# Performance work log

Measured on AMD Instinct MI355X. Metric: run time of the kernel, lower is better.

Reference implementation:

```python
import jax, jax.numpy as jnp
import numpy as np

F_DIM, H_DIM, B, T = 256, 512, 512, 128

def setup_inputs() -> dict:
    key = jax.random.key(0)
    ks = jax.random.split(key, 16)
    stdv_f = 1.0 / np.sqrt(F_DIM)
    stdv_h = 1.0 / np.sqrt(H_DIM)
    u = lambda k, shape, s: jax.random.uniform(k, shape, jnp.float32, -s, s)
    values = jax.random.normal(ks[0], (B, T, F_DIM), jnp.float32)
    delta = jax.random.uniform(ks[1], (B, T, F_DIM), jnp.float32) * 2.0
    masks = (jax.random.uniform(ks[2], (B, T, F_DIM)) < 0.8).astype(jnp.float32)
    inp = jnp.stack([values, delta, masks], axis=1)  # [B,3,T,F]
    return {
        'input': inp,
        # temp_decay_x (diag, F->F); mask buffer is unused in forward, faithful to source
        'Wdx': u(ks[3], (F_DIM, F_DIM), stdv_f), 'bdx': u(ks[4], (F_DIM,), stdv_f),
        # temp_decay_h (F->H)
        'Wdh': u(ks[5], (H_DIM, F_DIM), stdv_h), 'bdh': u(ks[6], (H_DIM,), stdv_h),
        # output_layer (H->F)
        'Wout': u(ks[7], (F_DIM, H_DIM), stdv_h), 'bout': u(ks[8], (F_DIM,), stdv_h),
        'Wz': u(ks[9], (F_DIM, F_DIM), stdv_f), 'bz': u(ks[10], (F_DIM,), stdv_f),
        # beta_layer (2F->F)
        'Wbeta': u(ks[11], (F_DIM, 2 * F_DIM), stdv_f), 'bbeta': u(ks[12], (F_DIM,), stdv_f),
        # GRUCell (2F -> H): weight_ih [3H,2F], weight_hh [3H,H]
        'Wih': u(ks[13], (3 * H_DIM, 2 * F_DIM), stdv_h),
        'Whh': u(ks[14], (3 * H_DIM, H_DIM), stdv_h),
        'bih': u(ks[15], (3 * H_DIM,), stdv_h),
        'bhh': u(jax.random.fold_in(key, 99), (3 * H_DIM,), stdv_h),
    }

def _mae(v, hat, m):
    return jnp.sum(jnp.abs(v - hat) * m) / (jnp.sum(m) + 1e-5)

def _forward(inp, Wdx, bdx, Wdh, bdh, Wout, bout, Wz, bz, Wbeta, bbeta, Wih, Whh, bih, bhh):
    values = jnp.transpose(inp[:, 0], (1, 0, 2))  # [T,B,F]
    delta = jnp.transpose(inp[:, 1], (1, 0, 2))
    masks = jnp.transpose(inp[:, 2], (1, 0, 2))
    H = Whh.shape[1]
    Wz_masked = Wz * (1.0 - jnp.eye(Wz.shape[0], dtype=Wz.dtype))

    def step(carry, xs):
        hid, loss = carry
        v, d, m = xs  # each [B,F]
        gamma_x = jnp.exp(-jax.nn.relu(d @ Wdx.T + bdx))
        gamma_h = jnp.exp(-jax.nn.relu(d @ Wdh.T + bdh))
        hid = hid * gamma_h
        x_hat = hid @ Wout.T + bout
        loss = loss + _mae(v, x_hat, m)
        x_c = m * v + (1.0 - m) * x_hat
        z_hat = x_c @ Wz_masked.T + bz
        loss = loss + _mae(v, z_hat, m)
        beta = jnp.concatenate([gamma_x, m], axis=1) @ Wbeta.T + bbeta
        c_hat = beta * z_hat + (1.0 - beta) * x_hat
        loss = loss + _mae(v, c_hat, m)
        c_c = m * v + (1.0 - m) * c_hat
        gi = jnp.concatenate([c_c, m], axis=1)  # [B,2F]
        gl = gi @ Wih.T + bih   # [B,3H]
        hl = hid @ Whh.T + bhh  # [B,3H]
        r = jax.nn.sigmoid(gl[:, :H] + hl[:, :H])
        z = jax.nn.sigmoid(gl[:, H:2 * H] + hl[:, H:2 * H])
        n = jnp.tanh(gl[:, 2 * H:] + r * hl[:, 2 * H:])
        hid = (1.0 - z) * n + z * hid
        return (hid, loss), (c_hat, c_c)

    hid0 = jnp.zeros((values.shape[1], H), dtype=inp.dtype)
    (_, x_loss), (c_hat_seq, c_c_seq) = jax.lax.scan(step, (hid0, jnp.float32(0.0)), (values, delta, masks))
    c_hat_list = jnp.transpose(c_hat_seq, (1, 0, 2))   # [B,T,F]
    imputations = jnp.transpose(c_c_seq, (1, 0, 2))    # [B,T,F]
    return c_hat_list, imputations, x_loss

def reference(input, Wdx, bdx, Wdh, bdh, Wout, bout, Wz, bz, Wbeta, bbeta, Wih, Whh, bih, bhh):
    return _forward(input, Wdx, bdx, Wdh, bdh, Wout, bout, Wz, bz, Wbeta, bbeta, Wih, Whh, bih, bhh)
```

## Files before the change

kernel.cpp:

```cpp
#include <hip/hip_runtime.h>
#include <math.h>


#define F 256
#define H 512
#define B 512
#define T 128
#define TF 32768
#define S3TF 98304
#define BTF ((size_t)B * T * F)

typedef __attribute__((ext_vector_type(8))) short bf8;
typedef __attribute__((ext_vector_type(4))) float f4;
#define MFMA16 __builtin_amdgcn_mfma_f32_16x16x32_bf16

__device__ inline short f2bf(float x) {
    unsigned u = __builtin_bit_cast(unsigned, x);
    u += 0x7fff + ((u >> 16) & 1);
    return (short)(u >> 16);
}
__device__ inline float bf2f(short s) {
    unsigned u = ((unsigned)(unsigned short)s) << 16;
    return __builtin_bit_cast(float, u);
}
__device__ inline float wsum(float v) {
#pragma unroll
    for (int o = 32; o > 0; o >>= 1) v += __shfl_down(v, o, 64);
    return v;
}

__global__ void init_k(float* __restrict__ hf, short* __restrict__ hb,
                       float* __restrict__ nd) {
    int i = blockIdx.x * 256 + threadIdx.x;
    hf[i] = 0.f; hb[i] = 0;
    if (i < 512) nd[i] = 0.f;
}

__global__ void wconv_k(const float* __restrict__ Wdx, const float* __restrict__ Wdh,
                        const float* __restrict__ Wz, const float* __restrict__ Wout,
                        const float* __restrict__ Wbeta, const float* __restrict__ Wih,
                        const float* __restrict__ Whh, short* __restrict__ wb) {
    int i = blockIdx.x * 256 + threadIdx.x;
    float v;
    if (i < 65536) v = Wdx[i];
    else if (i < 196608) v = Wdh[i - 65536];
    else if (i < 262144) { int l = i - 196608; v = ((l >> 8) == (l & 255)) ? 0.f : Wz[l]; }
    else if (i < 393216) v = Wout[i - 262144];
    else if (i < 524288) v = Wbeta[i - 393216];
    else if (i < 1310720) v = Wih[i - 524288];
    else v = Whh[i - 1310720];
    wb[i] = f2bf(v);
}

__global__ void aconv_k(const float* __restrict__ inp, short* __restrict__ dbf,
                        short* __restrict__ abf, float* __restrict__ den) {
    int i = blockIdx.x * 256 + threadIdx.x;
    int r = i >> 8, f = i & 255;
    int t = r >> 9, b = r & 511;
    const float* base = inp + (size_t)b * S3TF + (size_t)t * F;
    dbf[i] = f2bf(base[TF + f]);
    float m = base[2 * TF + f];
    abf[(size_t)r * 512 + 256 + f] = f2bf(m);
    float s = wsum(m);
    __shared__ float red[4];
    if ((threadIdx.x & 63) == 0) red[threadIdx.x >> 6] = s;
    __syncthreads();
    if (threadIdx.x == 0) atomicAdd(&den[t], red[0] + red[1] + red[2] + red[3]);
}

__global__ __launch_bounds__(256) void gx_gemm(const short* __restrict__ A,
                                               const short* __restrict__ W,
                                               const float* __restrict__ bias,
                                               short* __restrict__ abf) {
    int gw = blockIdx.x * 4 + (threadIdx.x >> 6);
    int lane = threadIdx.x & 63, l16 = lane & 15, quad = lane >> 4;
    int r0 = (gw >> 4) * 16, n0 = (gw & 15) * 16;
    const short* ar = A + (size_t)(r0 + l16) * 256 + quad * 8;
    const short* br = W + (size_t)(n0 + l16) * 256 + quad * 8;
    f4 acc = {};
#pragma unroll
    for (int k = 0; k < 256; k += 32)
        acc = MFMA16(*(const bf8*)(ar + k), *(const bf8*)(br + k), acc, 0, 0, 0);
    int n = n0 + l16;
    float bs = bias[n];
#pragma unroll
    for (int r = 0; r < 4; r++) {
        int row = r0 + quad * 4 + r;
        abf[(size_t)row * 512 + n] = f2bf(expf(-fmaxf(acc[r] + bs, 0.f)));
    }
}

__global__ __launch_bounds__(256) void gh_gemm(const short* __restrict__ A,
                                               const short* __restrict__ W,
                                               const float* __restrict__ bias,
                                               short* __restrict__ ghb) {
    int gw = blockIdx.x * 4 + (threadIdx.x >> 6);
    int lane = threadIdx.x & 63, l16 = lane & 15, quad = lane >> 4;
    int r0 = (gw >> 5) * 16, n0 = (gw & 31) * 16;
    const short* ar = A + (size_t)(r0 + l16) * 256 + quad * 8;
    const short* br = W + (size_t)(n0 + l16) * 256 + quad * 8;
    f4 acc = {};
#pragma unroll
    for (int k = 0; k < 256; k += 32)
        acc = MFMA16(*(const bf8*)(ar + k), *(const bf8*)(br + k), acc, 0, 0, 0);
    int n = n0 + l16;
    float bs = bias[n];
#pragma unroll
    for (int r = 0; r < 4; r++) {
        int row = r0 + quad * 4 + r;
        ghb[(size_t)row * 512 + n] = f2bf(expf(-fmaxf(acc[r] + bs, 0.f)));
    }
}

__global__ __launch_bounds__(256) void beta_gemm(const short* __restrict__ A,
                                                 const short* __restrict__ W,
                                                 const float* __restrict__ bias,
                                                 short* __restrict__ betab) {
    int gw = blockIdx.x * 4 + (threadIdx.x >> 6);
    int lane = threadIdx.x & 63, l16 = lane & 15, quad = lane >> 4;
    int r0 = (gw >> 4) * 16, n0 = (gw & 15) * 16;
    const short* ar = A + (size_t)(r0 + l16) * 512 + quad * 8;
    const short* br = W + (size_t)(n0 + l16) * 512 + quad * 8;
    f4 acc = {};
#pragma unroll
    for (int k = 0; k < 512; k += 32)
        acc = MFMA16(*(const bf8*)(ar + k), *(const bf8*)(br + k), acc, 0, 0, 0);
    int n = n0 + l16;
    float bs = bias[n];
#pragma unroll
    for (int r = 0; r < 4; r++) {
        int row = r0 + quad * 4 + r;
        betab[(size_t)row * 256 + n] = f2bf(acc[r] + bs);
    }
}

__global__ __launch_bounds__(256) void k1(const short* __restrict__ hidb,
                                          const short* __restrict__ Wo,
                                          const float* __restrict__ bout,
                                          const float* __restrict__ inp,
                                          short* __restrict__ xhatb,
                                          short* __restrict__ xcb,
                                          float* __restrict__ num, int t) {
    int gw = blockIdx.x * 4 + (threadIdx.x >> 6);
    int lane = threadIdx.x & 63, l16 = lane & 15, quad = lane >> 4;
    int b0 = (gw >> 4) * 16, n0 = (gw & 15) * 16;
    const short* ar = hidb + (size_t)(b0 + l16) * 512 + quad * 8;
    const short* br = Wo + (size_t)(n0 + l16) * 512 + quad * 8;
    f4 acc = {};
#pragma unroll
    for (int k = 0; k < 512; k += 32)
        acc = MFMA16(*(const bf8*)(ar + k), *(const bf8*)(br + k), acc, 0, 0, 0);
    int n = n0 + l16;
    float bs = bout[n];
    float l1 = 0.f;
#pragma unroll
    for (int r = 0; r < 4; r++) {
        int b = b0 + quad * 4 + r;
        const float* vb = inp + (size_t)b * S3TF + (size_t)t * F + n;
        float v = vb[0], m = vb[2 * TF];
        float xh = acc[r] + bs;
        l1 += fabsf(v - xh) * m;
        xhatb[(size_t)b * 256 + n] = f2bf(xh);
        xcb[(size_t)b * 256 + n] = f2bf(m * v + (1.f - m) * xh);
    }
    l1 = wsum(l1);
    __shared__ float red[4];
    if (lane == 0) red[threadIdx.x >> 6] = l1;
    __syncthreads();
    if (threadIdx.x == 0) atomicAdd(&num[t], red[0] + red[1] + red[2] + red[3]);
}

__global__ __launch_bounds__(256) void k2(const short* __restrict__ xcb,
                                          const short* __restrict__ Wzm,
                                          const float* __restrict__ bz,
                                          const short* __restrict__ xhatb,
                                          const short* __restrict__ betab,
                                          const float* __restrict__ inp,
                                          float* __restrict__ out,
                                          short* __restrict__ gib,
                                          float* __restrict__ num, int t) {
    int gw = blockIdx.x * 4 + (threadIdx.x >> 6);
    int lane = threadIdx.x & 63, l16 = lane & 15, quad = lane >> 4;
    int b0 = (gw >> 4) * 16, n0 = (gw & 15) * 16;
    const short* ar = xcb + (size_t)(b0 + l16) * 256 + quad * 8;
    const short* br = Wzm + (size_t)(n0 + l16) * 256 + quad * 8;
    f4 acc = {};
#pragma unroll
    for (int k = 0; k < 256; k += 32)
        acc = MFMA16(*(const bf8*)(ar + k), *(const bf8*)(br + k), acc, 0, 0, 0);
    int n = n0 + l16;
    float bs = bz[n];
    float l2 = 0.f, l3 = 0.f;
#pragma unroll
    for (int r = 0; r < 4; r++) {
        int b = b0 + quad * 4 + r;
        const float* vb = inp + (size_t)b * S3TF + (size_t)t * F + n;
        float v = vb[0], m = vb[2 * TF];
        float zh = acc[r] + bs;
        float xh = bf2f(xhatb[(size_t)b * 256 + n]);
        float bt = bf2f(betab[((size_t)t * 512 + b) * 256 + n]);
        float ch = bt * zh + (1.f - bt) * xh;
        float cc = m * v + (1.f - m) * ch;
        out[(size_t)b * TF + (size_t)t * F + n] = ch;
        out[BTF + (size_t)b * TF + (size_t)t * F + n] = cc;
        gib[(size_t)b * 512 + n] = f2bf(cc);
        gib[(size_t)b * 512 + 256 + n] = f2bf(m);
        l2 += fabsf(v - zh) * m;
        l3 += fabsf(v - ch) * m;
    }
    l2 = wsum(l2); l3 = wsum(l3);
    __shared__ float red2[2][4];
    if (lane == 0) { red2[0][threadIdx.x >> 6] = l2; red2[1][threadIdx.x >> 6] = l3; }
    __syncthreads();
    if (threadIdx.x == 0) {
        atomicAdd(&num[128 + t], red2[0][0] + red2[0][1] + red2[0][2] + red2[0][3]);
        atomicAdd(&num[256 + t], red2[1][0] + red2[1][1] + red2[1][2] + red2[1][3]);
    }
}

__global__ __launch_bounds__(256) void k3(const short* __restrict__ gib,
                                          const short* __restrict__ hidb,
                                          const float* __restrict__ hidf,
                                          const short* __restrict__ Wih,
                                          const short* __restrict__ Whh,
                                          const float* __restrict__ bih,
                                          const float* __restrict__ bhh,
                                          const short* __restrict__ ghb,
                                          float* __restrict__ hidf_n,
                                          short* __restrict__ hidb_n, int t) {
    int gw = blockIdx.x * 4 + (threadIdx.x >> 6);
    int lane = threadIdx.x & 63, l16 = lane & 15, quad = lane >> 4;
    int b0 = (gw >> 5) * 16, j0 = (gw & 31) * 16;
    const short* ag = gib + (size_t)(b0 + l16) * 512 + quad * 8;
    const short* ah = hidb + (size_t)(b0 + l16) * 512 + quad * 8;
    const short* w0 = Wih + (size_t)(j0 + l16) * 512 + quad * 8;
    const short* w3 = Whh + (size_t)(j0 + l16) * 512 + quad * 8;
    f4 aglr = {}, aglz = {}, agln = {}, ahlr = {}, ahlz = {}, ahln = {};
#pragma unroll
    for (int k = 0; k < 512; k += 32) {
        bf8 g = *(const bf8*)(ag + k);
        bf8 h = *(const bf8*)(ah + k);
        aglr = MFMA16(g, *(const bf8*)(w0 + k), aglr, 0, 0, 0);
        aglz = MFMA16(g, *(const bf8*)(w0 + 512 * 512 + k), aglz, 0, 0, 0);
        agln = MFMA16(g, *(const bf8*)(w0 + 1024 * 512 + k), agln, 0, 0, 0);
        ahlr = MFMA16(h, *(const bf8*)(w3 + k), ahlr, 0, 0, 0);
        ahlz = MFMA16(h, *(const bf8*)(w3 + 512 * 512 + k), ahlz, 0, 0, 0);
        ahln = MFMA16(h, *(const bf8*)(w3 + 1024 * 512 + k), ahln, 0, 0, 0);
    }
    int j = j0 + l16;
    float br = bih[j], bzg = bih[512 + j], bn = bih[1024 + j];
    float cr = bhh[j], czg = bhh[512 + j], cn = bhh[1024 + j];
#pragma unroll
    for (int r = 0; r < 4; r++) {
        int b = b0 + quad * 4 + r;
        float rg = 1.f / (1.f + expf(-(aglr[r] + br + ahlr[r] + cr)));
        float zg = 1.f / (1.f + expf(-(aglz[r] + bzg + ahlz[r] + czg)));
        float ng = tanhf(agln[r] + bn + rg * (ahln[r] + cn));
        float hold = hidf[(size_t)b * 512 + j];
        float hn = (1.f - zg) * ng + zg * hold;
        if (t + 1 < T) hn *= bf2f(ghb[((size_t)(t + 1) * 512 + b) * 512 + j]);
        hidf_n[(size_t)b * 512 + j] = hn;
        hidb_n[(size_t)b * 512 + j] = f2bf(hn);
    }
}

__global__ void final_k(const float* __restrict__ nd, float* __restrict__ outloss) {
    int tid = threadIdx.x;
    float v = (nd[tid] + nd[128 + tid] + nd[256 + tid]) / (nd[384 + tid] + 1e-5f);
    __shared__ float red[128];
    red[tid] = v; __syncthreads();
    for (int o = 64; o > 0; o >>= 1) { if (tid < o) red[tid] += red[tid + o]; __syncthreads(); }
    if (tid == 0) *outloss = red[0];
}

extern "C" void kernel_launch(void* const* d_in, const int* in_sizes, int n_in,
                              void* d_out, int out_size, void* d_ws, size_t ws_size,
                              hipStream_t stream) {
    const float* inp   = (const float*)d_in[0];
    const float* Wdx   = (const float*)d_in[1];
    const float* bdx   = (const float*)d_in[2];
    const float* Wdh   = (const float*)d_in[3];
    const float* bdh   = (const float*)d_in[4];
    const float* Wout  = (const float*)d_in[5];
    const float* bout  = (const float*)d_in[6];
    const float* Wz    = (const float*)d_in[7];
    const float* bz    = (const float*)d_in[8];
    const float* Wbeta = (const float*)d_in[9];
    const float* bbeta = (const float*)d_in[10];
    const float* Wih   = (const float*)d_in[11];
    const float* Whh   = (const float*)d_in[12];
    const float* bih   = (const float*)d_in[13];
    const float* bhh   = (const float*)d_in[14];
    float* out = (float*)d_out;

    char* p = (char*)d_ws;
    short* wb    = (short*)p; p += (size_t)2097152 * 2;
    short* dbf   = (short*)p; p += (size_t)16777216 * 2;
    short* abf   = (short*)p; p += (size_t)33554432 * 2;
    short* ghb   = (short*)p; p += (size_t)33554432 * 2;
    short* betab = (short*)p; p += (size_t)16777216 * 2;
    short* xhatb = (short*)p; p += (size_t)131072 * 2;
    short* xcb   = (short*)p; p += (size_t)131072 * 2;
    short* gib   = (short*)p; p += (size_t)262144 * 2;
    short* hbA   = (short*)p; p += (size_t)262144 * 2;
    short* hbB   = (short*)p; p += (size_t)262144 * 2;
    float* hfA   = (float*)p; p += (size_t)262144 * 4;
    float* hfB   = (float*)p; p += (size_t)262144 * 4;
    float* nd    = (float*)p; p += (size_t)512 * 4;

    const short* Wdxb   = wb;
    const short* Wdhb   = wb + 65536;
    const short* Wzmb   = wb + 196608;
    const short* Woutb  = wb + 262144;
    const short* Wbetab = wb + 393216;
    const short* Wihb   = wb + 524288;
    const short* Whhb   = wb + 1310720;

    init_k<<<1024, 256, 0, stream>>>(hfA, hbA, nd);
    wconv_k<<<8192, 256, 0, stream>>>(Wdx, Wdh, Wz, Wout, Wbeta, Wih, Whh, wb);
    aconv_k<<<65536, 256, 0, stream>>>(inp, dbf, abf, nd + 384);
    gx_gemm<<<16384, 256, 0, stream>>>(dbf, Wdxb, bdx, abf);
    gh_gemm<<<32768, 256, 0, stream>>>(dbf, Wdhb, bdh, ghb);
    beta_gemm<<<16384, 256, 0, stream>>>(abf, Wbetab, bbeta, betab);

    for (int t = 0; t < T; ++t) {
        short* hbc = (t & 1) ? hbB : hbA;
        short* hbn = (t & 1) ? hbA : hbB;
        float* hfc = (t & 1) ? hfB : hfA;
        float* hfn = (t & 1) ? hfA : hfB;
        k1<<<128, 256, 0, stream>>>(hbc, Woutb, bout, inp, xhatb, xcb, nd, t);
        k2<<<128, 256, 0, stream>>>(xcb, Wzmb, bz, xhatb, betab, inp, out, gib, nd, t);
        k3<<<256, 256, 0, stream>>>(gib, hbc, hfc, Wihb, Whhb, bih, bhh, ghb, hfn, hbn, t);
    }
    final_k<<<1, 128, 0, stream>>>(nd, out + 2 * BTF);
}
```

Before: 5.413 ms.

## Fuse recurrent steps into a persistent kernel with software grid barriers

Replaces the 384 per-timestep launches (k1, k2, k3) with one persistent 256-block kernel that loops over time and synchronises through a global atomic barrier. Within each step, the first 32 blocks fuse the output-layer and z-layer GEMMs, passing x_c through swizzled LDS instead of global memory. The GRU stage then reads the mask half directly from the precomputed buffer. Loss atomics become deterministic per-block partials reduced in a final kernel. This removes launch overhead and intermediate traffic, but leaves 224 blocks idle during the first phase, and the spin barrier assumes all 256 blocks are co-resident.

```diff
diff --git a/kernel.cpp b/kernel.cpp
--- a/kernel.cpp
+++ b/kernel.cpp
@@ -9,6 +9,7 @@
 #define TF 32768
 #define S3TF 98304
 #define BTF ((size_t)B * T * F)
+#define NBLK 256
 
 typedef __attribute__((ext_vector_type(8))) short bf8;
 typedef __attribute__((ext_vector_type(4))) float f4;
@@ -29,11 +30,29 @@
     return v;
 }
 
+__device__ inline void gbar(unsigned* cnt, unsigned* gen) {
+    __syncthreads();
+    if (threadIdx.x == 0) {
+        unsigned g = __hip_atomic_load(gen, __ATOMIC_RELAXED, __HIP_MEMORY_SCOPE_AGENT);
+        __threadfence();
+        unsigned a = __hip_atomic_fetch_add(cnt, 1u, __ATOMIC_ACQ_REL, __HIP_MEMORY_SCOPE_AGENT);
+        if (a == NBLK - 1) {
+            __hip_atomic_store(cnt, 0u, __ATOMIC_RELAXED, __HIP_MEMORY_SCOPE_AGENT);
+            __hip_atomic_store(gen, g + 1u, __ATOMIC_RELEASE, __HIP_MEMORY_SCOPE_AGENT);
+        } else {
+            while (__hip_atomic_load(gen, __ATOMIC_RELAXED, __HIP_MEMORY_SCOPE_AGENT) == g)
+                __builtin_amdgcn_s_sleep(1);
+        }
+        __threadfence();
+    }
+    __syncthreads();
+}
+
 __global__ void init_k(float* __restrict__ hf, short* __restrict__ hb,
-                       float* __restrict__ nd) {
+                       unsigned* __restrict__ bar) {
     int i = blockIdx.x * 256 + threadIdx.x;
     hf[i] = 0.f; hb[i] = 0;
-    if (i < 512) nd[i] = 0.f;
+    if (blockIdx.x == 0 && threadIdx.x < 32) bar[threadIdx.x] = 0u;
 }
 
 __global__ void wconv_k(const float* __restrict__ Wdx, const float* __restrict__ Wdh,
@@ -53,7 +72,7 @@
 }
 
 __global__ void aconv_k(const float* __restrict__ inp, short* __restrict__ dbf,
-                        short* __restrict__ abf, float* __restrict__ den) {
+                        short* __restrict__ abf, float* __restrict__ denP) {
     int i = blockIdx.x * 256 + threadIdx.x;
     int r = i >> 8, f = i & 255;
     int t = r >> 9, b = r & 511;
@@ -65,7 +84,7 @@
     __shared__ float red[4];
     if ((threadIdx.x & 63) == 0) red[threadIdx.x >> 6] = s;
     __syncthreads();
-    if (threadIdx.x == 0) atomicAdd(&den[t], red[0] + red[1] + red[2] + red[3]);
+    if (threadIdx.x == 0) denP[r] = red[0] + red[1] + red[2] + red[3];
 }
 
 __global__ __launch_bounds__(256) void gx_gemm(const short* __restrict__ A,
@@ -134,141 +153,184 @@
     }
 }
 
-__global__ __launch_bounds__(256) void k1(const short* __restrict__ hidb,
-                                          const short* __restrict__ Wo,
-                                          const float* __restrict__ bout,
-                                          const float* __restrict__ inp,
-                                          short* __restrict__ xhatb,
-                                          short* __restrict__ xcb,
-                                          float* __restrict__ num, int t) {
-    int gw = blockIdx.x * 4 + (threadIdx.x >> 6);
-    int lane = threadIdx.x & 63, l16 = lane & 15, quad = lane >> 4;
-    int b0 = (gw >> 4) * 16, n0 = (gw & 15) * 16;
-    const short* ar = hidb + (size_t)(b0 + l16) * 512 + quad * 8;
-    const short* br = Wo + (size_t)(n0 + l16) * 512 + quad * 8;
-    f4 acc = {};
-#pragma unroll
-    for (int k = 0; k < 512; k += 32)
-        acc = MFMA16(*(const bf8*)(ar + k), *(const bf8*)(br + k), acc, 0, 0, 0);
-    int n = n0 + l16;
-    float bs = bout[n];
-    float l1 = 0.f;
-#pragma unroll
-    for (int r = 0; r < 4; r++) {
-        int b = b0 + quad * 4 + r;
-        const float* vb = inp + (size_t)b * S3TF + (size_t)t * F + n;
-        float v = vb[0], m = vb[2 * TF];
-        float xh = acc[r] + bs;
-        l1 += fabsf(v - xh) * m;
-        xhatb[(size_t)b * 256 + n] = f2bf(xh);
-        xcb[(size_t)b * 256 + n] = f2bf(m * v + (1.f - m) * xh);
-    }
-    l1 = wsum(l1);
-    __shared__ float red[4];
-    if (lane == 0) red[threadIdx.x >> 6] = l1;
+struct LoopArgs {
+    const float* inp;
+    const short* Woutb; const float* bout;
+    const short* Wzmb;  const float* bz;
+    const short* betab; const short* abf; const short* ghb;
+    const short* Wihb;  const short* Whhb;
+    const float* bih;   const float* bhh;
+    short* gib;
+    float* out;
+    float* lossP;
+    short* hbA; short* hbB;
+    float* hfA; float* hfB;
+    unsigned* bar;
+};
+
+__global__ __launch_bounds__(256, 1) void loop_k(LoopArgs P) {
+    const int bc = blockIdx.x;
+    const int tid = threadIdx.x;
+    const int w = tid >> 6;
+    const int lane = tid & 63;
+    const int l16 = lane & 15;
+    const int quad = lane >> 4;
+
+    __shared__ short xcs[16 * 256];
+    __shared__ float redl[3][4];
+
+    const int jt = bc & 31, bg = bc >> 5;
+    const int j0 = jt * 16;
+    const int b0c = (bg * 4 + w) * 16;
+
+#pragma unroll 1
+    for (int t = 0; t < T; ++t) {
+        const short* hbc = (t & 1) ? P.hbB : P.hbA;
+        short* hbn = (t & 1) ? P.hbA : P.hbB;
+        const float* hfc = (t & 1) ? P.hfB : P.hfA;
+        float* hfn = (t & 1) ? P.hfA : P.hfB;
+
+        if (bc < 32) {
+            const int b0 = bc * 16;
+            f4 acc1[4] = {};
+            const short* ar = hbc + (size_t)(b0 + l16) * 512 + quad * 8;
+#pragma unroll
+            for (int k = 0; k < 512; k += 32) {
+                bf8 a = *(const bf8*)(ar + k);
+#pragma unroll
+                for (int nt = 0; nt < 4; nt++) {
+                    const short* wp = P.Woutb + (size_t)((w * 4 + nt) * 16 + l16) * 512 + quad * 8 + k;
+                    acc1[nt] = MFMA16(a, *(const bf8*)wp, acc1[nt], 0, 0, 0);
+                }
+            }
+            float l1 = 0.f;
+            f4 xhv[4], vv[4], mm[4];
+#pragma unroll
+            for (int nt = 0; nt < 4; nt++) {
+                int n = (w * 4 + nt) * 16 + l16;
+                float bs = P.bout[n];
+#pragma unroll
+                for (int r = 0; r < 4; r++) {
+                    int b = b0 + quad * 4 + r;
+                    const float* vb = P.inp + (size_t)b * S3TF + (size_t)t * F + n;
+                    float v = vb[0], m = vb[2 * TF];
+                    float xh = acc1[nt][r] + bs;
+                    l1 += fabsf(v - xh) * m;
+                    float xc = m * v + (1.f - m) * xh;
+                    int row = quad * 4 + r;
+                    *(short*)((char*)xcs + (row << 9) + (((unsigned)(n * 2)) ^ ((row & 7) << 4))) = f2bf(xc);
+                    xhv[nt][r] = xh; vv[nt][r] = v; mm[nt][r] = m;
+                }
+            }
+            __syncthreads();
+            f4 acc2[4] = {};
+#pragma unroll
+            for (int k = 0; k < 256; k += 32) {
+                bf8 a = *(const bf8*)((char*)xcs + (l16 << 9) +
+                                      (((unsigned)((k + quad * 8) * 2)) ^ ((l16 & 7) << 4)));
+#pragma unroll
+                for (int nt = 0; nt < 4; nt++) {
+                    const short* wp = P.Wzmb + (size_t)((w * 4 + nt) * 16 + l16) * 256 + quad * 8 + k;
+                    acc2[nt] = MFMA16(a, *(const bf8*)wp, acc2[nt], 0, 0, 0);
+                }
+            }
+            float l2 = 0.f, l3 = 0.f;
+#pragma unroll
+            for (int nt = 0; nt < 4; nt++) {
+                int n = (w * 4 + nt) * 16 + l16;
+                float bs = P.bz[n];
+#pragma unroll
+                for (int r = 0; r < 4; r++) {
+                    int b = b0 + quad * 4 + r;
+                    float zh = acc2[nt][r] + bs;
+                    float bt = bf2f(P.betab[((size_t)t * 512 + b) * 256 + n]);
+                    float xh = xhv[nt][r];
+                    float ch = bt * zh + (1.f - bt) * xh;
+                    float m = mm[nt][r], v = vv[nt][r];
+                    float cc = m * v + (1.f - m) * ch;
+                    P.out[(size_t)b * TF + (size_t)t * F + n] = ch;
+                    P.out[BTF + (size_t)b * TF + (size_t)t * F + n] = cc;
+                    P.gib[(size_t)b * 256 + n] = f2bf(cc);
+                    l2 += fabsf(v - zh) * m;
+                    l3 += fabsf(v - ch) * m;
+                }
+            }
+            l1 = wsum(l1); l2 = wsum(l2); l3 = wsum(l3);
+            if (lane == 0) { redl[0][w] = l1; redl[1][w] = l2; redl[2][w] = l3; }
+            __syncthreads();
+            if (tid == 0) {
+                float* lp = P.lossP + ((size_t)t * 32 + bc) * 3;
+                lp[0] = redl[0][0] + redl[0][1] + redl[0][2] + redl[0][3];
+                lp[1] = redl[1][0] + redl[1][1] + redl[1][2] + redl[1][3];
+                lp[2] = redl[2][0] + redl[2][1] + redl[2][2] + redl[2][3];
+            }
+        }
+        gbar(P.bar, P.bar + 16);
+
+        {
+            f4 aglr = {}, aglz = {}, agln = {}, ahlr = {}, ahlz = {}, ahln = {};
+            const short* ag = P.gib + (size_t)(b0c + l16) * 256 + quad * 8;
+            const short* am = P.abf + ((size_t)t * 512 + b0c + l16) * 512 + quad * 8;
+            const short* ah = hbc + (size_t)(b0c + l16) * 512 + quad * 8;
+            const short* w0 = P.Wihb + (size_t)(j0 + l16) * 512 + quad * 8;
+            const short* w3 = P.Whhb + (size_t)(j0 + l16) * 512 + quad * 8;
+#pragma unroll
+            for (int k = 0; k < 256; k += 32) {
+                bf8 g = *(const bf8*)(ag + k);
+                bf8 h = *(const bf8*)(ah + k);
+                aglr = MFMA16(g, *(const bf8*)(w0 + k), aglr, 0, 0, 0);
+                aglz = MFMA16(g, *(const bf8*)(w0 + 512 * 512 + k), aglz, 0, 0, 0);
+                agln = MFMA16(g, *(const bf8*)(w0 + 1024 * 512 + k), agln, 0, 0, 0);
+                ahlr = MFMA16(h, *(const bf8*)(w3 + k), ahlr, 0, 0, 0);
+                ahlz = MFMA16(h, *(const bf8*)(w3 + 512 * 512 + k), ahlz, 0, 0, 0);
+                ahln = MFMA16(h, *(const bf8*)(w3 + 1024 * 512 + k), ahln, 0, 0, 0);
+            }
+#pragma unroll
+            for (int k = 256; k < 512; k += 32) {
+                bf8 g = *(const bf8*)(am + k);
+                bf8 h = *(const bf8*)(ah + k);
+                aglr = MFMA16(g, *(const bf8*)(w0 + k), aglr, 0, 0, 0);
+                aglz = MFMA16(g, *(const bf8*)(w0 + 512 * 512 + k), aglz, 0, 0, 0);
+                agln = MFMA16(g, *(const bf8*)(w0 + 1024 * 512 + k), agln, 0, 0, 0);
+                ahlr = MFMA16(h, *(const bf8*)(w3 + k), ahlr, 0, 0, 0);
+                ahlz = MFMA16(h, *(const bf8*)(w3 + 512 * 512 + k), ahlz, 0, 0, 0);
+                ahln = MFMA16(h, *(const bf8*)(w3 + 1024 * 512 + k), ahln, 0, 0, 0);
+            }
+            int j = j0 + l16;
+            float br_ = P.bih[j], bzg = P.bih[512 + j], bn_ = P.bih[1024 + j];
+            float cr_ = P.bhh[j], czg = P.bhh[512 + j], cn_ = P.bhh[1024 + j];
+#pragma unroll
+            for (int r = 0; r < 4; r++) {
+                int b = b0c + quad * 4 + r;
+                float rg = 1.f / (1.f + expf(-(aglr[r] + br_ + ahlr[r] + cr_)));
+                float zg = 1.f / (1.f + expf(-(aglz[r] + bzg + ahlz[r] + czg)));
+                float ng = tanhf(agln[r] + bn_ + rg * (ahln[r] + cn_));
+                float hold = hfc[(size_t)b * 512 + j];
+                float hn = (1.f - zg) * ng + zg * hold;
+                if (t + 1 < T) hn *= bf2f(P.ghb[((size_t)(t + 1) * 512 + b) * 512 + j]);
+                hfn[(size_t)b * 512 + j] = hn;
+                hbn[(size_t)b * 512 + j] = f2bf(hn);
+            }
+        }
+        gbar(P.bar, P.bar + 16);
+    }
+}
+
+__global__ void final2_k(const float* __restrict__ lossP,
+                         const float* __restrict__ denP,
+                         float* __restrict__ outloss) {
+    int tid = threadIdx.x;
+    float n = 0.f;
+    for (int blk = 0; blk < 32; ++blk) {
+        const float* lp = lossP + ((size_t)tid * 32 + blk) * 3;
+        n += lp[0] + lp[1] + lp[2];
+    }
+    float d = 0.f;
+    const float* dp = denP + (size_t)tid * 512;
+    for (int b = 0; b < 512; ++b) d += dp[b];
+    __shared__ float red[128];
+    red[tid] = n / (d + 1e-5f);
     __syncthreads();
-    if (threadIdx.x == 0) atomicAdd(&num[t], red[0] + red[1] + red[2] + red[3]);
-}
-
-__global__ __launch_bounds__(256) void k2(const short* __restrict__ xcb,
-                                          const short* __restrict__ Wzm,
-                                          const float* __restrict__ bz,
-                                          const short* __restrict__ xhatb,
-                                          const short* __restrict__ betab,
-                                          const float* __restrict__ inp,
-                                          float* __restrict__ out,
-                                          short* __restrict__ gib,
-                                          float* __restrict__ num, int t) {
-    int gw = blockIdx.x * 4 + (threadIdx.x >> 6);
-    int lane = threadIdx.x & 63, l16 = lane & 15, quad = lane >> 4;
-    int b0 = (gw >> 4) * 16, n0 = (gw & 15) * 16;
-    const short* ar = xcb + (size_t)(b0 + l16) * 256 + quad * 8;
-    const short* br = Wzm + (size_t)(n0 + l16) * 256 + quad * 8;
-    f4 acc = {};
-#pragma unroll
-    for (int k = 0; k < 256; k += 32)
-        acc = MFMA16(*(const bf8*)(ar + k), *(const bf8*)(br + k), acc, 0, 0, 0);
-    int n = n0 + l16;
-    float bs = bz[n];
-    float l2 = 0.f, l3 = 0.f;
-#pragma unroll
-    for (int r = 0; r < 4; r++) {
-        int b = b0 + quad * 4 + r;
-        const float* vb = inp + (size_t)b * S3TF + (size_t)t * F + n;
-        float v = vb[0], m = vb[2 * TF];
-        float zh = acc[r] + bs;
-        float xh = bf2f(xhatb[(size_t)b * 256 + n]);
-        float bt = bf2f(betab[((size_t)t * 512 + b) * 256 + n]);
-        float ch = bt * zh + (1.f - bt) * xh;
-        float cc = m * v + (1.f - m) * ch;
-        out[(size_t)b * TF + (size_t)t * F + n] = ch;
-        out[BTF + (size_t)b * TF + (size_t)t * F + n] = cc;
-        gib[(size_t)b * 512 + n] = f2bf(cc);
-        gib[(size_t)b * 512 + 256 + n] = f2bf(m);
-        l2 += fabsf(v - zh) * m;
-        l3 += fabsf(v - ch) * m;
-    }
-    l2 = wsum(l2); l3 = wsum(l3);
-    __shared__ float red2[2][4];
-    if (lane == 0) { red2[0][threadIdx.x >> 6] = l2; red2[1][threadIdx.x >> 6] = l3; }
-    __syncthreads();
-    if (threadIdx.x == 0) {
-        atomicAdd(&num[128 + t], red2[0][0] + red2[0][1] + red2[0][2] + red2[0][3]);
-        atomicAdd(&num[256 + t], red2[1][0] + red2[1][1] + red2[1][2] + red2[1][3]);
-    }
-}
-
-__global__ __launch_bounds__(256) void k3(const short* __restrict__ gib,
-                                          const short* __restrict__ hidb,
-                                          const float* __restrict__ hidf,
-                                          const short* __restrict__ Wih,
-                                          const short* __restrict__ Whh,
-                                          const float* __restrict__ bih,
-                                          const float* __restrict__ bhh,
-                                          const short* __restrict__ ghb,
-                                          float* __restrict__ hidf_n,
-                                          short* __restrict__ hidb_n, int t) {
-    int gw = blockIdx.x * 4 + (threadIdx.x >> 6);
-    int lane = threadIdx.x & 63, l16 = lane & 15, quad = lane >> 4;
-    int b0 = (gw >> 5) * 16, j0 = (gw & 31) * 16;
-    const short* ag = gib + (size_t)(b0 + l16) * 512 + quad * 8;
-    const short* ah = hidb + (size_t)(b0 + l16) * 512 + quad * 8;
-    const short* w0 = Wih + (size_t)(j0 + l16) * 512 + quad * 8;
-    const short* w3 = Whh + (size_t)(j0 + l16) * 512 + quad * 8;
-    f4 aglr = {}, aglz = {}, agln = {}, ahlr = {}, ahlz = {}, ahln = {};
-#pragma unroll
-    for (int k = 0; k < 512; k += 32) {
-        bf8 g = *(const bf8*)(ag + k);
-        bf8 h = *(const bf8*)(ah + k);
-        aglr = MFMA16(g, *(const bf8*)(w0 + k), aglr, 0, 0, 0);
-        aglz = MFMA16(g, *(const bf8*)(w0 + 512 * 512 + k), aglz, 0, 0, 0);
-        agln = MFMA16(g, *(const bf8*)(w0 + 1024 * 512 + k), agln, 0, 0, 0);
-        ahlr = MFMA16(h, *(const bf8*)(w3 + k), ahlr, 0, 0, 0);
-        ahlz = MFMA16(h, *(const bf8*)(w3 + 512 * 512 + k), ahlz, 0, 0, 0);
-        ahln = MFMA16(h, *(const bf8*)(w3 + 1024 * 512 + k), ahln, 0, 0, 0);
-    }
-    int j = j0 + l16;
-    float br = bih[j], bzg = bih[512 + j], bn = bih[1024 + j];
-    float cr = bhh[j], czg = bhh[512 + j], cn = bhh[1024 + j];
-#pragma unroll
-    for (int r = 0; r < 4; r++) {
-        int b = b0 + quad * 4 + r;
-        float rg = 1.f / (1.f + expf(-(aglr[r] + br + ahlr[r] + cr)));
-        float zg = 1.f / (1.f + expf(-(aglz[r] + bzg + ahlz[r] + czg)));
-        float ng = tanhf(agln[r] + bn + rg * (ahln[r] + cn));
-        float hold = hidf[(size_t)b * 512 + j];
-        float hn = (1.f - zg) * ng + zg * hold;
-        if (t + 1 < T) hn *= bf2f(ghb[((size_t)(t + 1) * 512 + b) * 512 + j]);
-        hidf_n[(size_t)b * 512 + j] = hn;
-        hidb_n[(size_t)b * 512 + j] = f2bf(hn);
-    }
-}
-
-__global__ void final_k(const float* __restrict__ nd, float* __restrict__ outloss) {
-    int tid = threadIdx.x;
-    float v = (nd[tid] + nd[128 + tid] + nd[256 + tid]) / (nd[384 + tid] + 1e-5f);
-    __shared__ float red[128];
-    red[tid] = v; __syncthreads();
     for (int o = 64; o > 0; o >>= 1) { if (tid < o) red[tid] += red[tid + o]; __syncthreads(); }
     if (tid == 0) *outloss = red[0];
 }
@@ -299,14 +361,14 @@
     short* abf   = (short*)p; p += (size_t)33554432 * 2;
     short* ghb   = (short*)p; p += (size_t)33554432 * 2;
     short* betab = (short*)p; p += (size_t)16777216 * 2;
-    short* xhatb = (short*)p; p += (size_t)131072 * 2;
-    short* xcb   = (short*)p; p += (size_t)131072 * 2;
-    short* gib   = (short*)p; p += (size_t)262144 * 2;
+    short* gib   = (short*)p; p += (size_t)131072 * 2;
     short* hbA   = (short*)p; p += (size_t)262144 * 2;
     short* hbB   = (short*)p; p += (size_t)262144 * 2;
     float* hfA   = (float*)p; p += (size_t)262144 * 4;
     float* hfB   = (float*)p; p += (size_t)262144 * 4;
-    float* nd    = (float*)p; p += (size_t)512 * 4;
+    float* lossP = (float*)p; p += (size_t)12288 * 4;
+    float* denP  = (float*)p; p += (size_t)65536 * 4;
+    unsigned* bar = (unsigned*)p; p += (size_t)64 * 4;
 
     const short* Wdxb   = wb;
     const short* Wdhb   = wb + 65536;
@@ -316,21 +378,21 @@
     const short* Wihb   = wb + 524288;
     const short* Whhb   = wb + 1310720;
 
-    init_k<<<1024, 256, 0, stream>>>(hfA, hbA, nd);
+    init_k<<<1024, 256, 0, stream>>>(hfA, hbA, bar);
     wconv_k<<<8192, 256, 0, stream>>>(Wdx, Wdh, Wz, Wout, Wbeta, Wih, Whh, wb);
-    aconv_k<<<65536, 256, 0, stream>>>(inp, dbf, abf, nd + 384);
+    aconv_k<<<65536, 256, 0, stream>>>(inp, dbf, abf, denP);
     gx_gemm<<<16384, 256, 0, stream>>>(dbf, Wdxb, bdx, abf);
     gh_gemm<<<32768, 256, 0, stream>>>(dbf, Wdhb, bdh, ghb);
     beta_gemm<<<16384, 256, 0, stream>>>(abf, Wbetab, bbeta, betab);
 
-    for (int t = 0; t < T; ++t) {
-        short* hbc = (t & 1) ? hbB : hbA;
-        short* hbn = (t & 1) ? hbA : hbB;
-        float* hfc = (t & 1) ? hfB : hfA;
-        float* hfn = (t & 1) ? hfA : hfB;
-        k1<<<128, 256, 0, stream>>>(hbc, Woutb, bout, inp, xhatb, xcb, nd, t);
-        k2<<<128, 256, 0, stream>>>(xcb, Wzmb, bz, xhatb, betab, inp, out, gib, nd, t);
-        k3<<<256, 256, 0, stream>>>(gib, hbc, hfc, Wihb, Whhb, bih, bhh, ghb, hfn, hbn, t);
-    }
-    final_k<<<1, 128, 0, stream>>>(nd, out + 2 * BTF);
-}
+    LoopArgs la;
+    la.inp = inp; la.Woutb = Woutb; la.bout = bout;
+    la.Wzmb = Wzmb; la.bz = bz;
+    la.betab = betab; la.abf = abf; la.ghb = ghb;
+    la.Wihb = Wihb; la.Whhb = Whhb; la.bih = bih; la.bhh = bhh;
+    la.gib = gib; la.out = out; la.lossP = lossP;
+    la.hbA = hbA; la.hbB = hbB; la.hfA = hfA; la.hfB = hfB;
+    la.bar = bar;
+    loop_k<<<NBLK, 256, 0, stream>>>(la);
+    final2_k<<<1, 128, 0, stream>>>(lossP, denP, out + 2 * BTF);
+}
```

Measured after the change: 11.69 ms. 116% more time.
